# Kernel tuning notes

Measured on AMD Instinct MI355X. Metric: run time of the kernel, lower is better.

The kernel has to match this reference:

```python
import jax, jax.numpy as jnp
import numpy as np

N_EMBD = 2048
N_HEAD = 16
KV_GROUP = 4
HEAD_DIM = N_EMBD // N_HEAD          # 128
N_KV = N_HEAD // KV_GROUP            # 4
KV_DIM = N_KV * HEAD_DIM             # 512
B, T = 2, 2048
ROPE_THETA = 1000000.0


def setup_inputs() -> dict:
    key = jax.random.key(0)
    k0, k1, k2 = jax.random.split(key, 3)
    x = jax.random.normal(k0, (B, T, N_EMBD), dtype=jnp.float32)
    # weights stored (in, out); matches torch Linear math up to a transpose of random init
    W_attn = jax.random.normal(k1, (N_EMBD, N_EMBD + 2 * KV_DIM), dtype=jnp.float32) * 0.02
    b_attn = jnp.zeros((N_EMBD + 2 * KV_DIM,), dtype=jnp.float32)
    W_proj = jax.random.normal(k2, (N_EMBD, N_EMBD), dtype=jnp.float32) * 0.02
    # realistic RoPE frequencies (Qwen-style theta)
    inv_freq = 1.0 / (ROPE_THETA ** (np.arange(0, HEAD_DIM, 2, dtype=np.float64) / HEAD_DIM))
    ang = np.outer(np.arange(T, dtype=np.float64), inv_freq)  # (T, HEAD_DIM//2)
    freqs_cos = jnp.asarray(np.cos(ang), dtype=jnp.float32)
    freqs_sin = jnp.asarray(np.sin(ang), dtype=jnp.float32)
    return {"x": x, "W_attn": W_attn, "b_attn": b_attn, "W_proj": W_proj,
            "freqs_cos": freqs_cos, "freqs_sin": freqs_sin}


def _rope_expand(x, cos, sin, kv_group):
    # x: (B, T, n_kv, hd); complex rotate interleaved pairs, then expand to n_kv*kv_group heads
    Bx, Tx, nh, hd = x.shape
    xf = x.astype(jnp.float32).reshape(Bx, Tx, nh, hd // 2, 2)
    a, b = xf[..., 0], xf[..., 1]
    c = cos[None, :, None, :]  # (1, T, 1, hd//2)
    s = sin[None, :, None, :]
    yr = a * c - b * s
    yi = a * s + b * c
    y = jnp.stack([yr, yi], axis=-1).reshape(Bx, Tx, nh, hd)
    y = jnp.broadcast_to(y[:, :, :, None, :], (Bx, Tx, nh, kv_group, hd))
    return y.reshape(Bx, Tx, nh * kv_group, hd).astype(x.dtype)


def reference(x, W_attn, b_attn, W_proj, freqs_cos, freqs_sin):
    Bx, Tx, E = x.shape
    hd = 2 * freqs_cos.shape[-1]
    n_q = E // hd
    kv_dim = (W_attn.shape[1] - E) // 2
    n_kv = kv_dim // hd
    g = n_q // n_kv

    qkv = x @ W_attn + b_attn  # (B, T, E + 2*kv_dim)
    q = qkv[..., :E].reshape(Bx, Tx, n_q, hd).transpose(0, 2, 1, 3)          # bhtd
    k = qkv[..., E:E + kv_dim].reshape(Bx, Tx, n_kv, hd)
    v = qkv[..., E + kv_dim:].reshape(Bx, Tx, n_kv, hd)
    # faithful to source: RoPE on K AND V (not Q), then GQA expand
    k = _rope_expand(k, freqs_cos, freqs_sin, g).transpose(0, 2, 1, 3)       # bhtd
    v = _rope_expand(v, freqs_cos, freqs_sin, g).transpose(0, 2, 1, 3)       # bhtd

    scale = 1.0 / jnp.sqrt(jnp.asarray(hd, dtype=x.dtype))
    scores = jnp.einsum('bhqd,bhkd->bhqk', q, k) * scale                     # (B, H, T, T)
    causal = jnp.tril(jnp.ones((Tx, Tx), dtype=bool))
    scores = jnp.where(causal, scores, jnp.asarray(-jnp.inf, scores.dtype))
    attn = jax.nn.softmax(scores, axis=-1)
    y = jnp.einsum('bhqk,bhkd->bhqd', attn, v)
    y = y.transpose(0, 2, 1, 3).reshape(Bx, Tx, E)
    return y @ W_proj  # c_proj, no bias
```

## Files before the change

### kernel.cpp

```cpp
#include <hip/hip_runtime.h>
#include <cstdint>
#include <cstddef>

#define T_SEQ 2048
#define B_SZ  2
#define EMB   2048
#define NH    16
#define NKV   4
#define HD    128
#define KVD   512
#define QKVN  3072
#define MROWS (B_SZ*T_SEQ)

typedef __bf16 bf16x8 __attribute__((ext_vector_type(8)));
typedef float  f32x4  __attribute__((ext_vector_type(4)));
typedef short  s16x8  __attribute__((ext_vector_type(8)));
typedef unsigned short u16;

__device__ __forceinline__ u16 f2b(float f) {
  uint32_t u = __builtin_bit_cast(uint32_t, f);
  u += 0x7fffu + ((u >> 16) & 1u);
  return (u16)(u >> 16);
}
__device__ __forceinline__ float b2f(u16 h) {
  return __builtin_bit_cast(float, (uint32_t)h << 16);
}
__device__ __forceinline__ bf16x8 ld_bf8(const u16* p) {
  return __builtin_bit_cast(bf16x8, *(const s16x8*)p);
}
__device__ __forceinline__ void glds16(const void* g, void* l) {
  __builtin_amdgcn_global_load_lds((const __attribute__((address_space(1))) void*)g,
                                   (__attribute__((address_space(3))) void*)l, 16, 0, 0);
}
template<int N> __device__ __forceinline__ void waitv() {
  if constexpr (N == 0) asm volatile("s_waitcnt vmcnt(0)" ::: "memory");
  else if constexpr (N == 2) asm volatile("s_waitcnt vmcnt(2)" ::: "memory");
  else if constexpr (N == 3) asm volatile("s_waitcnt vmcnt(3)" ::: "memory");
  __builtin_amdgcn_sched_barrier(0);
}

__global__ void cvt_x_kernel(const float4* __restrict__ x, ushort4* __restrict__ xb, int n4) {
  int i = blockIdx.x*blockDim.x + threadIdx.x;
  if (i >= n4) return;
  float4 v = x[i];
  ushort4 o;
  o.x = f2b(v.x); o.y = f2b(v.y); o.z = f2b(v.z); o.w = f2b(v.w);
  xb[i] = o;
}

__global__ void transpose_w_kernel(const float* __restrict__ in, u16* __restrict__ out,
                                   int R, int C) {
  __shared__ float tile[64][65];
  int c0 = blockIdx.x*64, r0 = blockIdx.y*64;
  int tx = threadIdx.x, ty = threadIdx.y;
#pragma unroll
  for (int k = 0; k < 4; ++k) {
    int r = ty + k*16;
    float4 v = *(const float4*)&in[(size_t)(r0+r)*C + c0 + tx*4];
    tile[r][tx*4+0] = v.x; tile[r][tx*4+1] = v.y;
    tile[r][tx*4+2] = v.z; tile[r][tx*4+3] = v.w;
  }
  __syncthreads();
#pragma unroll
  for (int k = 0; k < 4; ++k) {
    int c = ty + k*16;
    ushort4 o;
    o.x = f2b(tile[tx*4+0][c]);
    o.y = f2b(tile[tx*4+1][c]);
    o.z = f2b(tile[tx*4+2][c]);
    o.w = f2b(tile[tx*4+3][c]);
    *(ushort4*)&out[(size_t)(c0+c)*R + r0 + tx*4] = o;
  }
}

template<int BN, int WGN, int MF, int NF, int NF1, int SB, int SB1, int VMC, bool BF16_OUT>
__global__ __launch_bounds__(512, 2) void gemm_kernel(const u16* __restrict__ A,
        const u16* __restrict__ Bt, const float* __restrict__ bias,
        void* __restrict__ Cout, int M, int N, int K) {
  constexpr int MF2 = MF/2;
  __shared__ u16 As[2][256*64];
  __shared__ u16 Bs[2][BN*64];
  const int tid = threadIdx.x;
  const int w = tid >> 6, lane = tid & 63;
  const int quad = lane >> 4, lc = lane & 15;
  const int wrow = w / WGN, wcol = w % WGN;
  const int gx = gridDim.x;
  const int lin = blockIdx.y*gx + blockIdx.x;
  const int swz = (lin & 7)*32 + (lin >> 3);
  const int m0 = (swz / gx)*256, n0 = (swz % gx)*BN;

  f32x4 acc[MF][NF] = {};
  bf16x8 af[MF2][2], bfv[NF][2];

  int xoff[2];
#pragma unroll
  for (int ks = 0; ks < 2; ++ks) xoff[ks] = ((ks*4 + quad) ^ (lc & 7))*8;
  const int arow0 = (wrow*MF*16 + lc)*64;
  const int brow0 = (wcol*NF*16 + lc)*64;

  const int srb  = tid >> 3;
  const int spos = (tid & 7) ^ (srb & 7);
  const u16* sAp = A  + (size_t)(m0 + srb)*K + spos*8;
  const u16* sBp = Bt + (size_t)(n0 + srb)*K + spos*8;

#define STAGE_A(bf_, t_, h_) do { \
    glds16(sAp + (size_t)((h_)*2  )*64*K + (size_t)(t_)*64, &As[bf_][((h_)*2  )*4096 + w*512]); \
    glds16(sAp + (size_t)((h_)*2+1)*64*K + (size_t)(t_)*64, &As[bf_][((h_)*2+1)*4096 + w*512]); \
  } while (0)
#define STAGE_B(bf_, t_, p_) do { \
    _Pragma("unroll") for (int r = (p_) ? SB1 : 0; r < ((p_) ? SB : SB1); ++r) \
      glds16(sBp + (size_t)r*64*K + (size_t)(t_)*64, &Bs[bf_][r*4096 + w*512]); \
  } while (0)
#define LDAH(S_, h_) do { _Pragma("unroll") for (int i = 0; i < MF2; ++i) { \
    af[i][0] = ld_bf8((S_) + arow0 + ((h_)*MF2 + i)*1024 + xoff[0]); \
    af[i][1] = ld_bf8((S_) + arow0 + ((h_)*MF2 + i)*1024 + xoff[1]); } } while (0)
#define LDBG(S_, g_) do { _Pragma("unroll") for (int j = (g_) ? NF1 : 0; j < ((g_) ? NF : NF1); ++j) { \
    bfv[j][0] = ld_bf8((S_) + brow0 + j*1024 + xoff[0]); \
    bfv[j][1] = ld_bf8((S_) + brow0 + j*1024 + xoff[1]); } } while (0)
#define CL(h_, g_) do { _Pragma("unroll") for (int ks = 0; ks < 2; ++ks) \
    _Pragma("unroll") for (int i = 0; i < MF2; ++i) \
    _Pragma("unroll") for (int j = (g_) ? NF1 : 0; j < ((g_) ? NF : NF1); ++j) \
      acc[(h_)*MF2+i][j] = __builtin_amdgcn_mfma_f32_16x16x32_bf16( \
          af[i][ks], bfv[j][ks], acc[(h_)*MF2+i][j], 0, 0, 0); } while (0)
#define BARX()  __builtin_amdgcn_s_barrier()
#define SCHB()  __builtin_amdgcn_sched_barrier(0)
#define MFMAPH(h_, g_) do { BARX(); \
    asm volatile("s_waitcnt lgkmcnt(0)" ::: "memory"); SCHB(); \
    __builtin_amdgcn_s_setprio(1); CL(h_, g_); __builtin_amdgcn_s_setprio(0); \
  } while (0)

  const int NT = K >> 6;
  STAGE_B(0, 0, 0); STAGE_B(0, 0, 1);
  STAGE_A(0, 0, 0); STAGE_A(0, 0, 1);
  STAGE_B(1, 1, 0); STAGE_B(1, 1, 1);
  waitv<VMC>();
  BARX(); SCHB();

  for (int t0 = 0; t0 < NT-2; t0 += 2) {
    const u16 *a0 = As[0], *b0 = Bs[0], *a1 = As[1], *b1 = Bs[1];
    LDAH(a0, 0); LDBG(b0, 0); STAGE_A(1, t0+1, 0);
    MFMAPH(0, 0); BARX();
    LDBG(b0, 1); STAGE_A(1, t0+1, 1);
    MFMAPH(0, 1); BARX();
    LDAH(a0, 1); STAGE_B(0, t0+2, 0);
    MFMAPH(1, 0); BARX();
    STAGE_B(0, t0+2, 1);
    MFMAPH(1, 1);
    waitv<VMC>();
    BARX(); SCHB();
    LDAH(a1, 0); LDBG(b1, 0); STAGE_A(0, t0+2, 0);
    MFMAPH(0, 0); BARX();
    LDBG(b1, 1); STAGE_A(0, t0+2, 1);
    MFMAPH(0, 1); BARX();
    LDAH(a1, 1); STAGE_B(1, t0+3, 0);
    MFMAPH(1, 0); BARX();
    STAGE_B(1, t0+3, 1);
    MFMAPH(1, 1);
    waitv<VMC>();
    BARX(); SCHB();
  }
  {
    const u16 *a0 = As[0], *b0 = Bs[0], *a1 = As[1], *b1 = Bs[1];
    LDAH(a0, 0); LDBG(b0, 0); STAGE_A(1, NT-1, 0);
    MFMAPH(0, 0); BARX();
    LDBG(b0, 1); STAGE_A(1, NT-1, 1);
    MFMAPH(0, 1); BARX();
    LDAH(a0, 1);
    MFMAPH(1, 0); BARX();
    MFMAPH(1, 1);
    waitv<0>();
    BARX(); SCHB();
    LDAH(a1, 0); LDBG(b1, 0);
    MFMAPH(0, 0); BARX();
    LDBG(b1, 1);
    MFMAPH(0, 1); BARX();
    LDAH(a1, 1);
    MFMAPH(1, 0); BARX();
    MFMAPH(1, 1);
  }

#undef STAGE_A
#undef STAGE_B
#undef LDAH
#undef LDBG
#undef CL
#undef BARX
#undef SCHB
#undef MFMAPH

#pragma unroll
  for (int j = 0; j < NF; ++j) {
    int col = n0 + wcol*NF*16 + j*16 + lc;
    float bv = BF16_OUT ? bias[col] : 0.0f;
#pragma unroll
    for (int i = 0; i < MF; ++i) {
      int rowb = m0 + wrow*MF*16 + i*16 + quad*4;
#pragma unroll
      for (int r = 0; r < 4; ++r) {
        float v = acc[i][j][r] + bv;
        if (BF16_OUT) ((u16*)Cout)[(size_t)(rowb+r)*N + col] = f2b(v);
        else          ((float*)Cout)[(size_t)(rowb+r)*N + col] = v;
      }
    }
  }
}

__global__ void rope_kernel(const u16* __restrict__ qkv, const float* __restrict__ fc,
                            const float* __restrict__ fs, u16* __restrict__ kout,
                            u16* __restrict__ vout) {
  int tid = threadIdx.x;
  int row = blockIdx.x;
  int i = tid & 63, kv = tid >> 6;
  int t = row & (T_SEQ-1);
  const u16* p = qkv + (size_t)row*QKVN + EMB + kv*HD + 2*i;
  float ka = b2f(p[0]),   kb = b2f(p[1]);
  float va = b2f(p[KVD]), vb = b2f(p[KVD+1]);
  float c = fc[t*64+i], s = fs[t*64+i];
  size_t ob = (size_t)row*KVD + kv*HD + 2*i;
  kout[ob]   = f2b(ka*c - kb*s);
  kout[ob+1] = f2b(ka*s + kb*c);
  vout[ob]   = f2b(va*c - vb*s);
  vout[ob+1] = f2b(va*s + vb*c);
}

__global__ void transpose_v_kernel(const u16* __restrict__ vb, u16* __restrict__ vtb) {
  __shared__ u16 tile[32][33];
  int bkv = blockIdx.z;
  int b = bkv >> 2, kv = bkv & 3;
  int d0 = blockIdx.y*32, t0 = blockIdx.x*32;
  int tx = threadIdx.x, ty = threadIdx.y;
#pragma unroll
  for (int i = 0; i < 32; i += 8)
    tile[ty+i][tx] = vb[(size_t)(b*T_SEQ + t0+ty+i)*KVD + kv*HD + d0 + tx];
  __syncthreads();
#pragma unroll
  for (int i = 0; i < 32; i += 8)
    vtb[(size_t)(bkv*HD + d0+ty+i)*T_SEQ + t0 + tx] = tile[tx][ty+i];
}

__global__ __launch_bounds__(256, 2) void flash_kernel(const u16* __restrict__ qkv,
    const u16* __restrict__ kb, const u16* __restrict__ vtb, u16* __restrict__ yb) {
  __shared__ u16 Ks[2][64*128];
  __shared__ u16 Vs[2][128*64];
  __shared__ u16 Ps[4][16*64];
  const int tid = threadIdx.x;
  const int w = tid >> 6, lane = tid & 63;
  const int quad = lane >> 4, lc = lane & 15;
  const int bkv = blockIdx.x & 7;
  const int r_  = blockIdx.x >> 3;
  const int b = bkv >> 2, kv = bkv & 3;
  const int h = kv*4 + w;
  const int qbase = (127 - r_)*16;

  bf16x8 qf[4];
  {
    const u16* qp = qkv + (size_t)(b*T_SEQ + qbase + lc)*QKVN + h*HD + quad*8;
#pragma unroll
    for (int ks = 0; ks < 4; ++ks) qf[ks] = ld_bf8(qp + ks*32);
  }

  f32x4 o[8] = {};
  float rs[4] = {0.f, 0.f, 0.f, 0.f};
  const u16* kbase = kb  + (size_t)b*T_SEQ*KVD + kv*HD;
  const u16* vbase = vtb + (size_t)bkv*HD*T_SEQ;
  const int nk = qbase + 16;
  const int nt = (nk + 63) >> 6;
  const float cs = 0.08838834764831845f * 1.4426950408889634f;
  u16* pw = Ps[w];

  const u16* kptr[4];
  const u16* vptr[4];
#pragma unroll
  for (int rr = 0; rr < 4; ++rr) {
    int krow = (rr*4 + w)*4 + (lane >> 4);
    int kcc  = (lane & 15) ^ (krow & 15);
    kptr[rr] = kbase + (size_t)krow*KVD + kcc*8;
    int vrow = (rr*4 + w)*8 + (lane >> 3);
    int vcc  = (lane & 7) ^ (vrow & 7);
    vptr[rr] = vbase + (size_t)vrow*T_SEQ + vcc*8;
  }

  int koff[4], voff[2], poff[2];
#pragma unroll
  for (int ks = 0; ks < 4; ++ks) koff[ks] = lc*128 + (((ks*4 + quad) ^ lc)*8);
#pragma unroll
  for (int ks = 0; ks < 2; ++ks) voff[ks] = lc*64 + (((ks*4 + quad) ^ (lc & 7))*8);
#pragma unroll
  for (int ks = 0; ks < 2; ++ks) poff[ks] = lc*64 + (((ks*4 + quad) ^ (lc & 7))*8);
  int pwb[4], pwx[4];
#pragma unroll
  for (int r = 0; r < 4; ++r) {
    pwb[r] = (quad*4 + r)*64 + (lc & 7);
    pwx[r] = (quad*4 + r) & 7;
  }
  const int pcc = lc >> 3;

#pragma unroll
  for (int rr = 0; rr < 4; ++rr) glds16(kptr[rr], &Ks[0][(rr*4 + w)*512]);
#pragma unroll
  for (int rr = 0; rr < 4; ++rr) glds16(vptr[rr], &Vs[0][(rr*4 + w)*512]);
  asm volatile("s_waitcnt vmcnt(0)" ::: "memory");
  __builtin_amdgcn_sched_barrier(0);
  __builtin_amdgcn_s_barrier();
  __builtin_amdgcn_sched_barrier(0);

  for (int t = 0; t < nt; ++t) {
    const int cur = t & 1;
    if (t + 1 < nt) {
#pragma unroll
      for (int rr = 0; rr < 4; ++rr)
        glds16(kptr[rr] + (size_t)(t+1)*64*KVD, &Ks[cur^1][(rr*4 + w)*512]);
#pragma unroll
      for (int rr = 0; rr < 4; ++rr)
        glds16(vptr[rr] + (size_t)(t+1)*64,     &Vs[cur^1][(rr*4 + w)*512]);
    }
    const u16* ksb = Ks[cur];
    const u16* vsb = Vs[cur];
    const int k0 = t*64;

    f32x4 sc[4] = {};
    __builtin_amdgcn_s_setprio(1);
#pragma unroll
    for (int nt2 = 0; nt2 < 4; ++nt2)
#pragma unroll
      for (int ks = 0; ks < 4; ++ks) {
        bf16x8 kf = ld_bf8(ksb + nt2*16*128 + koff[ks]);
        sc[nt2] = __builtin_amdgcn_mfma_f32_16x16x32_bf16(qf[ks], kf, sc[nt2], 0, 0, 0);
      }
    __builtin_amdgcn_s_setprio(0);

    if (k0 + 63 > qbase) {
#pragma unroll
      for (int nt2 = 0; nt2 < 4; ++nt2) {
        int key = k0 + nt2*16 + lc;
        int qrow = qbase + quad*4;
#pragma unroll
        for (int r = 0; r < 4; ++r) {
          float e = __builtin_amdgcn_exp2f(sc[nt2][r]*cs);
          float p = (key <= qrow + r) ? e : 0.0f;
          rs[r] += p;
          pw[pwb[r] + ((nt2*2 + pcc) ^ pwx[r])*8] = f2b(p);
        }
      }
    } else {
#pragma unroll
      for (int nt2 = 0; nt2 < 4; ++nt2)
#pragma unroll
        for (int r = 0; r < 4; ++r) {
          float p = __builtin_amdgcn_exp2f(sc[nt2][r]*cs);
          rs[r] += p;
          pw[pwb[r] + ((nt2*2 + pcc) ^ pwx[r])*8] = f2b(p);
        }
    }

    bf16x8 pa[2];
#pragma unroll
    for (int ks = 0; ks < 2; ++ks)
      pa[ks] = ld_bf8(pw + poff[ks]);

    __builtin_amdgcn_s_setprio(1);
#pragma unroll
    for (int j = 0; j < 8; ++j)
#pragma unroll
      for (int ks = 0; ks < 2; ++ks) {
        bf16x8 vf = ld_bf8(vsb + j*16*64 + voff[ks]);
        o[j] = __builtin_amdgcn_mfma_f32_16x16x32_bf16(pa[ks], vf, o[j], 0, 0, 0);
      }
    __builtin_amdgcn_s_setprio(0);

    asm volatile("s_waitcnt vmcnt(0)" ::: "memory");
    __builtin_amdgcn_sched_barrier(0);
    __builtin_amdgcn_s_barrier();
    __builtin_amdgcn_sched_barrier(0);
  }

#pragma unroll
  for (int r = 0; r < 4; ++r) {
    float v = rs[r];
#pragma unroll
    for (int off2 = 8; off2 >= 1; off2 >>= 1)
      v += __shfl_xor(v, off2);
    float inv = 1.0f / v;
    size_t orow = (size_t)(b*T_SEQ + qbase + quad*4 + r)*EMB + h*HD;
#pragma unroll
    for (int j = 0; j < 8; ++j)
      yb[orow + j*16 + lc] = f2b(o[j][r]*inv);
  }
}

extern "C" void kernel_launch(void* const* d_in, const int* in_sizes, int n_in,
                              void* d_out, int out_size, void* d_ws, size_t ws_size,
                              hipStream_t stream) {
  const float* x      = (const float*)d_in[0];
  const float* W_attn = (const float*)d_in[1];
  const float* b_attn = (const float*)d_in[2];
  const float* W_proj = (const float*)d_in[3];
  const float* fc     = (const float*)d_in[4];
  const float* fs     = (const float*)d_in[5];

  u16* ws   = (u16*)d_ws;
  u16* xb   = ws;
  u16* WaT  = xb   + (size_t)MROWS*EMB;
  u16* qkv  = WaT  + (size_t)QKVN*EMB;
  u16* kbuf = qkv  + (size_t)MROWS*QKVN;
  u16* vb   = kbuf + (size_t)MROWS*KVD;
  u16* vtb  = vb   + (size_t)MROWS*KVD;
  u16* WpT  = WaT;
  u16* yb   = xb;
  float* out = (float*)d_out;

  cvt_x_kernel<<<(MROWS*EMB/4 + 255)/256, 256, 0, stream>>>(
      (const float4*)x, (ushort4*)xb, MROWS*EMB/4);
  transpose_w_kernel<<<dim3(QKVN/64, EMB/64), dim3(16, 16), 0, stream>>>(
      W_attn, WaT, EMB, QKVN);
  gemm_kernel<192, 4, 8, 3, 2, 3, 2, 3, true>
      <<<dim3(QKVN/192, MROWS/256), 512, 0, stream>>>(
      xb, WaT, b_attn, qkv, MROWS, QKVN, EMB);
  rope_kernel<<<MROWS, 256, 0, stream>>>(qkv, fc, fs, kbuf, vb);
  transpose_v_kernel<<<dim3(T_SEQ/32, HD/32, B_SZ*NKV), dim3(32, 8), 0, stream>>>(vb, vtb);
  transpose_w_kernel<<<dim3(EMB/64, EMB/64), dim3(16, 16), 0, stream>>>(
      W_proj, WpT, EMB, EMB);
  flash_kernel<<<dim3(B_SZ*NKV*(T_SEQ/16)), 256, 0, stream>>>(qkv, kbuf, vtb, yb);
  gemm_kernel<128, 2, 4, 4, 2, 2, 1, 2, false>
      <<<dim3(EMB/128, MROWS/256), 512, 0, stream>>>(
      yb, WpT, nullptr, out, MROWS, EMB, EMB);
}
```

Before: 283.1 us.

## Pair causal query blocks per workgroup to share K/V tiles and balance load

Each flash-attention workgroup now handles two 16-row query blocks: a short one near the sequence start and its mirror near the end. Both share the same K/V shared-memory tiles for the key tiles they have in common, so the workgroup count halves. Per-workgroup work is now nearly equal across the causal triangle, and staged K/V loads are reused by two query blocks. In exchange, accumulator and Q-fragment registers double, which may hurt occupancy or cause spills under the two-block-per-SM launch bound, and each workgroup now runs longer.

```diff
diff --git a/kernel.cpp b/kernel.cpp
--- a/kernel.cpp
+++ b/kernel.cpp
@@ -250,21 +250,23 @@
   const int r_  = blockIdx.x >> 3;
   const int b = bkv >> 2, kv = bkv & 3;
   const int h = kv*4 + w;
-  const int qbase = (127 - r_)*16;
-
-  bf16x8 qf[4];
+  const int qbA = r_*16;
+  const int qbB = (127 - r_)*16;
+
+  bf16x8 qfA[4], qfB[4];
   {
-    const u16* qp = qkv + (size_t)(b*T_SEQ + qbase + lc)*QKVN + h*HD + quad*8;
-#pragma unroll
-    for (int ks = 0; ks < 4; ++ks) qf[ks] = ld_bf8(qp + ks*32);
-  }
-
-  f32x4 o[8] = {};
-  float rs[4] = {0.f, 0.f, 0.f, 0.f};
+    const u16* qpA = qkv + (size_t)(b*T_SEQ + qbA + lc)*QKVN + h*HD + quad*8;
+    const u16* qpB = qkv + (size_t)(b*T_SEQ + qbB + lc)*QKVN + h*HD + quad*8;
+#pragma unroll
+    for (int ks = 0; ks < 4; ++ks) { qfA[ks] = ld_bf8(qpA + ks*32); qfB[ks] = ld_bf8(qpB + ks*32); }
+  }
+
+  f32x4 oA[8] = {}, oB[8] = {};
+  float rsA[4] = {0.f,0.f,0.f,0.f}, rsB[4] = {0.f,0.f,0.f,0.f};
   const u16* kbase = kb  + (size_t)b*T_SEQ*KVD + kv*HD;
   const u16* vbase = vtb + (size_t)bkv*HD*T_SEQ;
-  const int nk = qbase + 16;
-  const int nt = (nk + 63) >> 6;
+  const int ntA = (qbA + 16 + 63) >> 6;
+  const int nt  = (qbB + 16 + 63) >> 6;
   const float cs = 0.08838834764831845f * 1.4426950408889634f;
   u16* pw = Ps[w];
 
@@ -304,6 +306,63 @@
   __builtin_amdgcn_s_barrier();
   __builtin_amdgcn_sched_barrier(0);
 
+#define SMAX(SC_, QB_, RS_) do { \
+    if (k0 + 63 > (QB_)) { \
+      _Pragma("unroll") for (int nt2 = 0; nt2 < 4; ++nt2) { \
+        int key = k0 + nt2*16 + lc; \
+        int qrow = (QB_) + quad*4; \
+        _Pragma("unroll") for (int r = 0; r < 4; ++r) { \
+          float e = __builtin_amdgcn_exp2f(SC_[nt2][r]*cs); \
+          float p = (key <= qrow + r) ? e : 0.0f; \
+          RS_[r] += p; \
+          pw[pwb[r] + ((nt2*2 + pcc) ^ pwx[r])*8] = f2b(p); \
+        } \
+      } \
+    } else { \
+      _Pragma("unroll") for (int nt2 = 0; nt2 < 4; ++nt2) \
+        _Pragma("unroll") for (int r = 0; r < 4; ++r) { \
+          float p = __builtin_amdgcn_exp2f(SC_[nt2][r]*cs); \
+          RS_[r] += p; \
+          pw[pwb[r] + ((nt2*2 + pcc) ^ pwx[r])*8] = f2b(p); \
+        } \
+    } \
+  } while (0)
+
+#define TILE_BODY(DOA_) do { \
+    f32x4 scB[4] = {}; f32x4 scA[4] = {}; \
+    __builtin_amdgcn_s_setprio(1); \
+    _Pragma("unroll") for (int nt2 = 0; nt2 < 4; ++nt2) { \
+      bf16x8 kf[4]; \
+      _Pragma("unroll") for (int ks = 0; ks < 4; ++ks) \
+        kf[ks] = ld_bf8(ksb + nt2*16*128 + koff[ks]); \
+      _Pragma("unroll") for (int ks = 0; ks < 4; ++ks) { \
+        scB[nt2] = __builtin_amdgcn_mfma_f32_16x16x32_bf16(qfB[ks], kf[ks], scB[nt2], 0, 0, 0); \
+        if (DOA_) scA[nt2] = __builtin_amdgcn_mfma_f32_16x16x32_bf16(qfA[ks], kf[ks], scA[nt2], 0, 0, 0); \
+      } \
+    } \
+    __builtin_amdgcn_s_setprio(0); \
+    SMAX(scB, qbB, rsB); \
+    bf16x8 paB[2]; \
+    _Pragma("unroll") for (int ks = 0; ks < 2; ++ks) paB[ks] = ld_bf8(pw + poff[ks]); \
+    bf16x8 paA[2]; \
+    if (DOA_) { \
+      SMAX(scA, qbA, rsA); \
+      _Pragma("unroll") for (int ks = 0; ks < 2; ++ks) paA[ks] = ld_bf8(pw + poff[ks]); \
+    } \
+    __builtin_amdgcn_s_setprio(1); \
+    _Pragma("unroll") for (int j = 0; j < 8; ++j) { \
+      bf16x8 vf0 = ld_bf8(vsb + j*16*64 + voff[0]); \
+      bf16x8 vf1 = ld_bf8(vsb + j*16*64 + voff[1]); \
+      oB[j] = __builtin_amdgcn_mfma_f32_16x16x32_bf16(paB[0], vf0, oB[j], 0, 0, 0); \
+      oB[j] = __builtin_amdgcn_mfma_f32_16x16x32_bf16(paB[1], vf1, oB[j], 0, 0, 0); \
+      if (DOA_) { \
+        oA[j] = __builtin_amdgcn_mfma_f32_16x16x32_bf16(paA[0], vf0, oA[j], 0, 0, 0); \
+        oA[j] = __builtin_amdgcn_mfma_f32_16x16x32_bf16(paA[1], vf1, oA[j], 0, 0, 0); \
+      } \
+    } \
+    __builtin_amdgcn_s_setprio(0); \
+  } while (0)
+
   for (int t = 0; t < nt; ++t) {
     const int cur = t & 1;
     if (t + 1 < nt) {
@@ -318,73 +377,32 @@
     const u16* vsb = Vs[cur];
     const int k0 = t*64;
 
-    f32x4 sc[4] = {};
-    __builtin_amdgcn_s_setprio(1);
-#pragma unroll
-    for (int nt2 = 0; nt2 < 4; ++nt2)
-#pragma unroll
-      for (int ks = 0; ks < 4; ++ks) {
-        bf16x8 kf = ld_bf8(ksb + nt2*16*128 + koff[ks]);
-        sc[nt2] = __builtin_amdgcn_mfma_f32_16x16x32_bf16(qf[ks], kf, sc[nt2], 0, 0, 0);
-      }
-    __builtin_amdgcn_s_setprio(0);
-
-    if (k0 + 63 > qbase) {
-#pragma unroll
-      for (int nt2 = 0; nt2 < 4; ++nt2) {
-        int key = k0 + nt2*16 + lc;
-        int qrow = qbase + quad*4;
-#pragma unroll
-        for (int r = 0; r < 4; ++r) {
-          float e = __builtin_amdgcn_exp2f(sc[nt2][r]*cs);
-          float p = (key <= qrow + r) ? e : 0.0f;
-          rs[r] += p;
-          pw[pwb[r] + ((nt2*2 + pcc) ^ pwx[r])*8] = f2b(p);
-        }
-      }
-    } else {
-#pragma unroll
-      for (int nt2 = 0; nt2 < 4; ++nt2)
-#pragma unroll
-        for (int r = 0; r < 4; ++r) {
-          float p = __builtin_amdgcn_exp2f(sc[nt2][r]*cs);
-          rs[r] += p;
-          pw[pwb[r] + ((nt2*2 + pcc) ^ pwx[r])*8] = f2b(p);
-        }
-    }
-
-    bf16x8 pa[2];
-#pragma unroll
-    for (int ks = 0; ks < 2; ++ks)
-      pa[ks] = ld_bf8(pw + poff[ks]);
-
-    __builtin_amdgcn_s_setprio(1);
-#pragma unroll
-    for (int j = 0; j < 8; ++j)
-#pragma unroll
-      for (int ks = 0; ks < 2; ++ks) {
-        bf16x8 vf = ld_bf8(vsb + j*16*64 + voff[ks]);
-        o[j] = __builtin_amdgcn_mfma_f32_16x16x32_bf16(pa[ks], vf, o[j], 0, 0, 0);
-      }
-    __builtin_amdgcn_s_setprio(0);
+    if (t < ntA) { TILE_BODY(1); } else { TILE_BODY(0); }
 
     asm volatile("s_waitcnt vmcnt(0)" ::: "memory");
     __builtin_amdgcn_sched_barrier(0);
     __builtin_amdgcn_s_barrier();
     __builtin_amdgcn_sched_barrier(0);
   }
+#undef TILE_BODY
+#undef SMAX
 
 #pragma unroll
   for (int r = 0; r < 4; ++r) {
-    float v = rs[r];
-#pragma unroll
-    for (int off2 = 8; off2 >= 1; off2 >>= 1)
-      v += __shfl_xor(v, off2);
-    float inv = 1.0f / v;
-    size_t orow = (size_t)(b*T_SEQ + qbase + quad*4 + r)*EMB + h*HD;
-#pragma unroll
-    for (int j = 0; j < 8; ++j)
-      yb[orow + j*16 + lc] = f2b(o[j][r]*inv);
+    float vA = rsA[r], vB = rsB[r];
+#pragma unroll
+    for (int off2 = 8; off2 >= 1; off2 >>= 1) {
+      vA += __shfl_xor(vA, off2);
+      vB += __shfl_xor(vB, off2);
+    }
+    float invA = 1.0f / vA, invB = 1.0f / vB;
+    size_t orowA = (size_t)(b*T_SEQ + qbA + quad*4 + r)*EMB + h*HD;
+    size_t orowB = (size_t)(b*T_SEQ + qbB + quad*4 + r)*EMB + h*HD;
+#pragma unroll
+    for (int j = 0; j < 8; ++j) {
+      yb[orowA + j*16 + lc] = f2b(oA[j][r]*invA);
+      yb[orowB + j*16 + lc] = f2b(oB[j][r]*invB);
+    }
   }
 }
 
@@ -420,7 +438,7 @@
   transpose_v_kernel<<<dim3(T_SEQ/32, HD/32, B_SZ*NKV), dim3(32, 8), 0, stream>>>(vb, vtb);
   transpose_w_kernel<<<dim3(EMB/64, EMB/64), dim3(16, 16), 0, stream>>>(
       W_proj, WpT, EMB, EMB);
-  flash_kernel<<<dim3(B_SZ*NKV*(T_SEQ/16)), 256, 0, stream>>>(qkv, kbuf, vtb, yb);
+  flash_kernel<<<dim3(B_SZ*NKV*(T_SEQ/32)), 256, 0, stream>>>(qkv, kbuf, vtb, yb);
   gemm_kernel<128, 2, 4, 4, 2, 2, 1, 2, false>
       <<<dim3(EMB/128, MROWS/256), 512, 0, stream>>>(
       yb, WpT, nullptr, out, MROWS, EMB, EMB);
```

Result: no change. 279.7 us (-1.2%).
